# Kernel optimization log

Measured on AMD Instinct MI355X. Metric: run time of the kernel, lower is better.

Reference implementation:

```python
import jax, jax.numpy as jnp
import numpy as np

B, L, S, H, E, D = 4, 2048, 2048, 8, 64, 64

def setup_inputs() -> dict:
    key = jax.random.key(0)
    kq, kk, kv = jax.random.split(key, 3)
    queries = jax.random.normal(kq, (B, L, H, E), dtype=jnp.float32)
    keys = jax.random.normal(kk, (B, S, H, E), dtype=jnp.float32)
    values = jax.random.normal(kv, (B, S, H, D), dtype=jnp.float32)
    return {"queries": queries, "keys": keys, "values": values}

def reference(queries, keys, values):
    # scale = self.scale or 1/sqrt(E)
    scale = 1.0 / jnp.sqrt(jnp.float32(queries.shape[-1]))
    # scores: [B, H, L, S]
    scores = jnp.einsum('blhe,bshe->bhls', queries, keys)
    # dropout is identity at inference (Keras Dropout only active in training)
    A = jax.nn.softmax(scale * scores, axis=-1)
    # output: [B, L, H, D]
    return jnp.einsum('bhls,bshd->blhd', A, values)
```

## Files before the change

kernel.cpp:

```cpp
#include <hip/hip_runtime.h>


#define B_ 4
#define L_ 2048
#define S_ 2048
#define H_ 8

#define NUMSZ (B_ * L_ * H_ * 64)
#define LSZ (B_ * L_ * H_)
#define KVELEM (B_ * H_ * S_ * 64)
#define TILE_ELEMS 2048

typedef __attribute__((ext_vector_type(8))) __bf16 bf16x8;
typedef __attribute__((ext_vector_type(4))) __bf16 bf16x4;
typedef __attribute__((ext_vector_type(16))) float floatx16;

union BF4U { bf16x4 v; uint2 u; };
union BF8U { bf16x8 v; uint4 u; };

__device__ __forceinline__ void async_load16(const void* g, void* l) {
  __builtin_amdgcn_global_load_lds(
      (const __attribute__((address_space(1))) unsigned int*)g,
      (__attribute__((address_space(3))) unsigned int*)l, 16, 0, 0);
}

__device__ __forceinline__ bf16x8 cvt8(float4 a, float4 b) {
  bf16x8 r;
  r[0] = (__bf16)a.x; r[1] = (__bf16)a.y; r[2] = (__bf16)a.z; r[3] = (__bf16)a.w;
  r[4] = (__bf16)b.x; r[5] = (__bf16)b.y; r[6] = (__bf16)b.z; r[7] = (__bf16)b.w;
  return r;
}

__device__ __forceinline__ void softmax_pb(const floatx16& sc, int h32, float& l,
                                           bf16x8& pB0v, bf16x8& pB1v) {
  BF4U pg[4];
#pragma unroll
  for (int g = 0; g < 4; ++g) {
    float p0 = __builtin_amdgcn_exp2f(sc[4 * g + 0]);
    float p1 = __builtin_amdgcn_exp2f(sc[4 * g + 1]);
    float p2 = __builtin_amdgcn_exp2f(sc[4 * g + 2]);
    float p3 = __builtin_amdgcn_exp2f(sc[4 * g + 3]);
    l += (p0 + p1) + (p2 + p3);
    pg[g].v = (bf16x4){(__bf16)p0, (__bf16)p1, (__bf16)p2, (__bf16)p3};
  }
  uint2 sendA = h32 ? pg[0].u : pg[1].u;
  uint2 sendB = h32 ? pg[2].u : pg[3].u;
  uint2 recvA, recvB;
  recvA.x = __shfl_xor((int)sendA.x, 32);
  recvA.y = __shfl_xor((int)sendA.y, 32);
  recvB.x = __shfl_xor((int)sendB.x, 32);
  recvB.y = __shfl_xor((int)sendB.y, 32);
  BF8U pB0, pB1;
  if (h32 == 0) {
    pB0.u = (uint4){pg[0].u.x, pg[0].u.y, recvA.x, recvA.y};
    pB1.u = (uint4){pg[2].u.x, pg[2].u.y, recvB.x, recvB.y};
  } else {
    pB0.u = (uint4){recvA.x, recvA.y, pg[1].u.x, pg[1].u.y};
    pB1.u = (uint4){recvB.x, recvB.y, pg[3].u.x, pg[3].u.y};
  }
  pB0v = pB0.v;
  pB1v = pB1.v;
}

__global__ __launch_bounds__(256) void prep_kernel(const float* __restrict__ K,
                                                   const float* __restrict__ V,
                                                   __bf16* __restrict__ Kb,
                                                   __bf16* __restrict__ Vb) {
  __shared__ float Vs[32 * 64];
  const int bid = blockIdx.x;
  const int tile = bid & 63;
  const int h = (bid >> 6) & 7;
  const int b = bid >> 9;
  const int s0 = tile * 32;
  const int i = threadIdx.x;

  {
    const int s = i >> 3, cp = i & 7;
    const int e0 = 8 * (cp ^ (s & 7));
    const float* src = K + (((size_t)(b * S_ + s0 + s) * H_ + h) * 64 + e0);
    float4 a = *(const float4*)src;
    float4 bb = *(const float4*)(src + 4);
    *(bf16x8*)(Kb + (size_t)bid * TILE_ELEMS + i * 8) = cvt8(a, bb);
  }
  {
    const int s = i >> 3, d0 = (i & 7) * 8;
    const float* src = V + (((size_t)(b * S_ + s0 + s) * H_ + h) * 64 + d0);
    float4 a = *(const float4*)src;
    float4 bb = *(const float4*)(src + 4);
    *(float4*)&Vs[s * 64 + d0] = a;
    *(float4*)&Vs[s * 64 + d0 + 4] = bb;
  }
  __syncthreads();
  {
    const int Ll = i >> 3, cp = i & 7;
    const int ci = cp ^ (Ll & 7);
    const int d = 2 * Ll + (ci >> 2);
    const int ch = ci & 3;
    BF8U o;
#pragma unroll
    for (int j = 0; j < 8; ++j) o.v[j] = (__bf16)Vs[(8 * ch + j) * 64 + d];
    *(bf16x8*)(Vb + (size_t)bid * TILE_ELEMS + i * 8) = o.v;
  }
}

__global__ __launch_bounds__(256, 2) void attn_kernel(const float* __restrict__ Q,
                                                      const __bf16* __restrict__ Kb,
                                                      const __bf16* __restrict__ Vb,
                                                      float* __restrict__ O,
                                                      float* __restrict__ num_ws,
                                                      float* __restrict__ l_ws,
                                                      int splits) {
  __shared__ __align__(16) __bf16 Kt[2][2 * TILE_ELEMS];
  __shared__ __align__(16) __bf16 Vt[2][2 * TILE_ELEMS];

  const int tid = threadIdx.x;
  const int lane = tid & 63;
  const int wave = tid >> 6;
  const int q32 = lane & 31;
  const int h32 = lane >> 5;

  const int bid = blockIdx.x;
  const int qb = bid & 7;
  const int h = (bid >> 3) & 7;
  const int b = (bid >> 6) & 3;
  const int split = bid >> 8;

  const int NT2 = (S_ / 32) / splits / 2;
  const int tile0 = split * NT2 * 2;

  const float qscale = 0.125f * 1.44269504088896340736f;
  const int qrow0 = qb * 256 + wave * 64 + q32;
  bf16x8 qf[2][4];
#pragma unroll
  for (int g = 0; g < 2; ++g) {
    const float* qp = Q + ((size_t)(b * L_ + qrow0 + g * 32) * H_ + h) * 64;
#pragma unroll
    for (int c = 0; c < 4; ++c) {
      const float* p = qp + c * 16 + h32 * 8;
      float4 a = *(const float4*)p;
      float4 bb = *(const float4*)(p + 4);
      float t[8] = {a.x, a.y, a.z, a.w, bb.x, bb.y, bb.z, bb.w};
#pragma unroll
      for (int j = 0; j < 8; ++j) qf[g][c][j] = (__bf16)(t[j] * qscale);
    }
  }

  int koff[4];
#pragma unroll
  for (int c = 0; c < 4; ++c) koff[c] = (q32 * 8 + (((2 * c + h32) ^ (q32 & 7)))) * 8;
  int voff[2][2];
#pragma unroll
  for (int s2 = 0; s2 < 2; ++s2)
#pragma unroll
    for (int dt = 0; dt < 2; ++dt) {
      int dp = dt * 32 + q32;
      int Ll = dp >> 1;
      int ci = (dp & 1) * 4 + 2 * s2 + h32;
      voff[s2][dt] = (Ll * 8 + (ci ^ (Ll & 7))) * 8;
    }

  float l[2] = {0.f, 0.f};
  floatx16 ot[2][2];
#pragma unroll
  for (int g = 0; g < 2; ++g)
#pragma unroll
    for (int r = 0; r < 16; ++r) { ot[g][0][r] = 0.f; ot[g][1][r] = 0.f; }

  const __bf16* KbBH = Kb + (size_t)((b * H_ + h) * 64) * TILE_ELEMS;
  const __bf16* VbBH = Vb + (size_t)((b * H_ + h) * 64) * TILE_ELEMS;
  const int lin8 = (wave * 64 + lane) * 8;

#pragma unroll
  for (int st = 0; st < 2; ++st) {
    async_load16(KbBH + (size_t)(tile0 + st) * TILE_ELEMS + lin8,
                 &Kt[0][st * TILE_ELEMS + wave * 512]);
    async_load16(VbBH + (size_t)(tile0 + st) * TILE_ELEMS + lin8,
                 &Vt[0][st * TILE_ELEMS + wave * 512]);
  }

  for (int t = 0; t < NT2; ++t) {
    const int buf = t & 1;
    __syncthreads();

    if (t + 1 < NT2) {
#pragma unroll
      for (int st = 0; st < 2; ++st) {
        async_load16(KbBH + (size_t)(tile0 + 2 * (t + 1) + st) * TILE_ELEMS + lin8,
                     &Kt[buf ^ 1][st * TILE_ELEMS + wave * 512]);
        async_load16(VbBH + (size_t)(tile0 + 2 * (t + 1) + st) * TILE_ELEMS + lin8,
                     &Vt[buf ^ 1][st * TILE_ELEMS + wave * 512]);
      }
    }

#pragma unroll
    for (int sb = 0; sb < 2; ++sb) {
      const __bf16* Kbuf = &Kt[buf][sb * TILE_ELEMS];
      const __bf16* Vbuf = &Vt[buf][sb * TILE_ELEMS];

      bf16x8 kA[4];
#pragma unroll
      for (int c = 0; c < 4; ++c) kA[c] = *(const bf16x8*)&Kbuf[koff[c]];

      floatx16 sc0, sc1;
#pragma unroll
      for (int r = 0; r < 16; ++r) { sc0[r] = 0.f; sc1[r] = 0.f; }
#pragma unroll
      for (int c = 0; c < 4; ++c)
        sc0 = __builtin_amdgcn_mfma_f32_32x32x16_bf16(kA[c], qf[0][c], sc0, 0, 0, 0);
#pragma unroll
      for (int c = 0; c < 4; ++c)
        sc1 = __builtin_amdgcn_mfma_f32_32x32x16_bf16(kA[c], qf[1][c], sc1, 0, 0, 0);

      bf16x8 p00, p01, p10, p11;
      softmax_pb(sc0, h32, l[0], p00, p01);
      softmax_pb(sc1, h32, l[1], p10, p11);

      bf16x8 vA[4];
      vA[0] = *(const bf16x8*)&Vbuf[voff[0][0]];
      vA[1] = *(const bf16x8*)&Vbuf[voff[0][1]];
      vA[2] = *(const bf16x8*)&Vbuf[voff[1][0]];
      vA[3] = *(const bf16x8*)&Vbuf[voff[1][1]];
      ot[0][0] = __builtin_amdgcn_mfma_f32_32x32x16_bf16(vA[0], p00, ot[0][0], 0, 0, 0);
      ot[0][1] = __builtin_amdgcn_mfma_f32_32x32x16_bf16(vA[1], p00, ot[0][1], 0, 0, 0);
      ot[1][0] = __builtin_amdgcn_mfma_f32_32x32x16_bf16(vA[0], p10, ot[1][0], 0, 0, 0);
      ot[1][1] = __builtin_amdgcn_mfma_f32_32x32x16_bf16(vA[1], p10, ot[1][1], 0, 0, 0);
      ot[0][0] = __builtin_amdgcn_mfma_f32_32x32x16_bf16(vA[2], p01, ot[0][0], 0, 0, 0);
      ot[0][1] = __builtin_amdgcn_mfma_f32_32x32x16_bf16(vA[3], p01, ot[0][1], 0, 0, 0);
      ot[1][0] = __builtin_amdgcn_mfma_f32_32x32x16_bf16(vA[2], p11, ot[1][0], 0, 0, 0);
      ot[1][1] = __builtin_amdgcn_mfma_f32_32x32x16_bf16(vA[3], p11, ot[1][1], 0, 0, 0);
    }
  }

#pragma unroll
  for (int g = 0; g < 2; ++g) {
    float lg = l[g] + __shfl_xor(l[g], 32);
    const int qrow = qrow0 + g * 32;
    if (splits == 1) {
      const float inv = 1.0f / lg;
      float* orow = O + ((size_t)(b * L_ + qrow) * H_ + h) * 64;
#pragma unroll
      for (int dt = 0; dt < 2; ++dt)
#pragma unroll
        for (int gg = 0; gg < 4; ++gg) {
          float4 v = {ot[g][dt][4 * gg + 0] * inv, ot[g][dt][4 * gg + 1] * inv,
                      ot[g][dt][4 * gg + 2] * inv, ot[g][dt][4 * gg + 3] * inv};
          *(float4*)(orow + dt * 32 + gg * 8 + h32 * 4) = v;
        }
    } else {
      float* nrow =
          num_ws + (size_t)split * NUMSZ + ((size_t)(b * L_ + qrow) * H_ + h) * 64;
#pragma unroll
      for (int dt = 0; dt < 2; ++dt)
#pragma unroll
        for (int gg = 0; gg < 4; ++gg) {
          float4 v = {ot[g][dt][4 * gg + 0], ot[g][dt][4 * gg + 1],
                      ot[g][dt][4 * gg + 2], ot[g][dt][4 * gg + 3]};
          *(float4*)(nrow + dt * 32 + gg * 8 + h32 * 4) = v;
        }
      if (h32 == 0)
        l_ws[(size_t)split * LSZ + (size_t)(b * L_ + qrow) * H_ + h] = lg;
    }
  }
}

__global__ __launch_bounds__(256) void combine_kernel(const float* __restrict__ num_ws,
                                                      const float* __restrict__ l_ws,
                                                      float* __restrict__ O, int splits) {
  const size_t i4 = ((size_t)blockIdx.x * 256 + threadIdx.x) * 4;
  float4 acc = {0.f, 0.f, 0.f, 0.f};
  float lt = 0.f;
  for (int s = 0; s < splits; ++s) {
    float4 v = *(const float4*)(num_ws + (size_t)s * NUMSZ + i4);
    acc.x += v.x; acc.y += v.y; acc.z += v.z; acc.w += v.w;
    lt += l_ws[(size_t)s * LSZ + (i4 >> 6)];
  }
  const float inv = 1.0f / lt;
  float4 o = {acc.x * inv, acc.y * inv, acc.z * inv, acc.w * inv};
  *(float4*)(O + i4) = o;
}

extern "C" void kernel_launch(void* const* d_in, const int* in_sizes, int n_in,
                              void* d_out, int out_size, void* d_ws, size_t ws_size,
                              hipStream_t stream) {
  const float* Q = (const float*)d_in[0];
  const float* K = (const float*)d_in[1];
  const float* V = (const float*)d_in[2];
  float* O = (float*)d_out;

  __bf16* Kb = (__bf16*)d_ws;
  __bf16* Vb = Kb + KVELEM;
  float* num_ws = (float*)(Vb + KVELEM);
  const size_t base = (size_t)2 * KVELEM * sizeof(__bf16);
  const size_t per_split = ((size_t)NUMSZ + (size_t)LSZ) * sizeof(float);
  int splits = 1;
  if (ws_size >= base + 2 * per_split) splits = 2;
  float* l_ws = num_ws + (size_t)splits * NUMSZ;

  prep_kernel<<<B_ * H_ * 64, 256, 0, stream>>>(K, V, Kb, Vb);
  dim3 grid(B_ * H_ * (L_ / 256) * splits);
  attn_kernel<<<grid, 256, 0, stream>>>(Q, Kb, Vb, O, num_ws, l_ws, splits);
  if (splits > 1) {
    combine_kernel<<<NUMSZ / 4 / 256, 256, 0, stream>>>(num_ws, l_ws, O, splits);
  }
}
```

Baseline: 144.3 us.

## Remap blocks so each XCD owns whole (b,h) pairs, raise splits and occupancy

Block indices in both the prep and attention kernels are remapped so that all blocks touching a given (batch, head) K/V slice land on the same XCD, which is meant to improve L2 reuse of the converted bf16 K/V tiles. The attention kernel's launch bounds go from 2 to 4 blocks per CU, and the KV dimension is split four ways when the workspace allows. This gives more parallel blocks at the cost of a larger combine pass and tighter register budgets, which may cause spills.

```diff
diff --git a/kernel.cpp b/kernel.cpp
--- a/kernel.cpp
+++ b/kernel.cpp
@@ -68,9 +68,13 @@
                                                    __bf16* __restrict__ Vb) {
   __shared__ float Vs[32 * 64];
   const int bid = blockIdx.x;
-  const int tile = bid & 63;
-  const int h = (bid >> 6) & 7;
-  const int b = bid >> 9;
+  const int xcd = bid & 7;
+  const int idx = bid >> 3;
+  const int pair = xcd * 4 + (idx >> 6);
+  const int tile = idx & 63;
+  const int h = pair & 7;
+  const int b = pair >> 3;
+  const int obid = pair * 64 + tile;
   const int s0 = tile * 32;
   const int i = threadIdx.x;
 
@@ -80,7 +84,7 @@
     const float* src = K + (((size_t)(b * S_ + s0 + s) * H_ + h) * 64 + e0);
     float4 a = *(const float4*)src;
     float4 bb = *(const float4*)(src + 4);
-    *(bf16x8*)(Kb + (size_t)bid * TILE_ELEMS + i * 8) = cvt8(a, bb);
+    *(bf16x8*)(Kb + (size_t)obid * TILE_ELEMS + i * 8) = cvt8(a, bb);
   }
   {
     const int s = i >> 3, d0 = (i & 7) * 8;
@@ -99,11 +103,11 @@
     BF8U o;
 #pragma unroll
     for (int j = 0; j < 8; ++j) o.v[j] = (__bf16)Vs[(8 * ch + j) * 64 + d];
-    *(bf16x8*)(Vb + (size_t)bid * TILE_ELEMS + i * 8) = o.v;
-  }
-}
-
-__global__ __launch_bounds__(256, 2) void attn_kernel(const float* __restrict__ Q,
+    *(bf16x8*)(Vb + (size_t)obid * TILE_ELEMS + i * 8) = o.v;
+  }
+}
+
+__global__ __launch_bounds__(256, 4) void attn_kernel(const float* __restrict__ Q,
                                                       const __bf16* __restrict__ Kb,
                                                       const __bf16* __restrict__ Vb,
                                                       float* __restrict__ O,
@@ -120,10 +124,16 @@
   const int h32 = lane >> 5;
 
   const int bid = blockIdx.x;
-  const int qb = bid & 7;
-  const int h = (bid >> 3) & 7;
-  const int b = (bid >> 6) & 3;
-  const int split = bid >> 8;
+  const int xcd = bid & 7;
+  const int idx = bid >> 3;
+  const int bs = 8 * splits;
+  const int pairl = idx / bs;
+  const int sub = idx - pairl * bs;
+  const int pair = xcd * 4 + pairl;
+  const int qb = sub & 7;
+  const int split = sub >> 3;
+  const int h = pair & 7;
+  const int b = pair >> 3;
 
   const int NT2 = (S_ / 32) / splits / 2;
   const int tile0 = split * NT2 * 2;
@@ -166,8 +176,8 @@
 #pragma unroll
     for (int r = 0; r < 16; ++r) { ot[g][0][r] = 0.f; ot[g][1][r] = 0.f; }
 
-  const __bf16* KbBH = Kb + (size_t)((b * H_ + h) * 64) * TILE_ELEMS;
-  const __bf16* VbBH = Vb + (size_t)((b * H_ + h) * 64) * TILE_ELEMS;
+  const __bf16* KbBH = Kb + (size_t)(pair * 64) * TILE_ELEMS;
+  const __bf16* VbBH = Vb + (size_t)(pair * 64) * TILE_ELEMS;
   const int lin8 = (wave * 64 + lane) * 8;
 
 #pragma unroll
@@ -293,7 +303,8 @@
   const size_t base = (size_t)2 * KVELEM * sizeof(__bf16);
   const size_t per_split = ((size_t)NUMSZ + (size_t)LSZ) * sizeof(float);
   int splits = 1;
-  if (ws_size >= base + 2 * per_split) splits = 2;
+  if (ws_size >= base + 4 * per_split) splits = 4;
+  else if (ws_size >= base + 2 * per_split) splits = 2;
   float* l_ws = num_ws + (size_t)splits * NUMSZ;
 
   prep_kernel<<<B_ * H_ * 64, 256, 0, stream>>>(K, V, Kb, Vb);
```

New measurement: 399.4 us. +176.8%, slower.
